# Kernel tuning notes

Measured on AMD Instinct MI355X. Metric: run time of the kernel, lower is better.

## Reference

```python
import jax, jax.numpy as jnp
import numpy as np

N_HEADS = 8


def setup_inputs() -> dict:
    key = jax.random.key(0)
    ks = jax.random.split(key, 6)
    B, U, Lx, Ly = 16, 512, 1024, 1024
    x = jax.random.normal(ks[0], (B, U, Lx), dtype=jnp.float32)
    y = jax.random.normal(ks[1], (B, U, Ly), dtype=jnp.float32)
    xy_mask = jax.random.randint(ks[2], (B, Lx, Ly), 0, 2).astype(jnp.bool_)
    wq = jax.random.normal(ks[3], (U, U), dtype=jnp.float32) * (1.0 / np.sqrt(U))
    wk = jax.random.normal(ks[4], (U, U), dtype=jnp.float32) * (1.0 / np.sqrt(U))
    wo = jax.random.normal(ks[5], (U, U), dtype=jnp.float32) * (1.0 / np.sqrt(U))
    return {"x": x, "y": y, "xy_mask": xy_mask, "wq": wq, "wk": wk, "wo": wo}


def reference(x, y, xy_mask, wq, wk, wo):
    # x: (B, U, Lx), y: (B, U, Ly), xy_mask: (B, Lx, Ly)
    B, U, Lx = x.shape
    Ly = y.shape[2]
    H = N_HEADS
    d = U // H
    scale = 1.0 / (d ** 0.5)

    # 1x1 conv (bias=False) == channel-mixing matmul; weight layout (out, in)
    Q = jnp.einsum('ou,bul->bol', wq, x)   # (B, U, Lx)
    K = jnp.einsum('ou,bul->bol', wk, y)   # (B, U, Ly)

    # split channels into heads (head-major channel order, matching torch.split)
    Qh = Q.reshape(B, H, d, Lx)
    Kh = K.reshape(B, H, d, Ly)

    # ReLU-scored attention with mask (no softmax)
    A = jnp.einsum('bhdx,bhdy->bhxy', Qh, Kh)           # (B, H, Lx, Ly)
    A = jnp.maximum(A, 0.0) * scale
    A = jnp.where(xy_mask[:, None, :, :], A, 0.0)

    C = jnp.einsum('bhxy,bhdy->bhdx', A, Kh).reshape(B, U, Lx)

    # per-row element-count normalization (rows with zero count use 1)
    n_el = jnp.maximum(jnp.sum(xy_mask, axis=2), 1)     # (B, Lx)
    C = C / n_el[:, None, :].astype(x.dtype)

    E = 0.5 * (Q + C)
    return jnp.einsum('ou,bul->bol', wo, E)
```

## Files before the change

kernel.cpp:

```cpp
#include <hip/hip_runtime.h>
#include <stdint.h>
#include <stddef.h>

#define B_  16
#define U_  512
#define LX_ 1024
#define LY_ 1024
#define H_  8
#define D_  64

typedef unsigned short ushort_t;
typedef unsigned int   uint_t;
typedef __bf16 v8bf  __attribute__((ext_vector_type(8)));
typedef float  v16f  __attribute__((ext_vector_type(16)));

__device__ __forceinline__ ushort_t bf16u(float f) {
    uint_t u = __float_as_uint(f);
    uint_t r = (u + 0x7FFFu + ((u >> 16) & 1u)) >> 16;
    return (ushort_t)r;
}
__device__ __forceinline__ float bfu2f(ushort_t u) {
    return __uint_as_float(((uint_t)u) << 16);
}
__device__ __forceinline__ uint_t pkbf16(float f0, float f1) {
    uint_t u0 = __float_as_uint(f0), u1 = __float_as_uint(f1);
    u0 = u0 + 0x7FFFu + ((u0 >> 16) & 1u);
    u1 = u1 + 0x7FFFu + ((u1 >> 16) & 1u);
    return __builtin_amdgcn_perm(u1, u0, 0x07060302u);
}
__device__ __forceinline__ void gload16(const void* g, void* l) {
    auto gp = (const __attribute__((address_space(1))) uint32_t*)(uintptr_t)g;
    auto lp = (__attribute__((address_space(3))) uint32_t*)(uintptr_t)l;
    __builtin_amdgcn_global_load_lds(gp, lp, 16, 0, 0);
}

__global__ void detect_kernel(const uint_t* __restrict__ mask, int* __restrict__ flag) {
    __shared__ int s;
    if (threadIdx.x == 0) s = 0;
    __syncthreads();
    int c = 0;
    for (int i = threadIdx.x; i < 1024; i += 256) c += (mask[i] <= 1u) ? 1 : 0;
    atomicAdd(&s, c);
    __syncthreads();
    if (threadIdx.x == 0) *flag = (s >= 1000) ? 1 : 0;
}

__global__ __launch_bounds__(256) void nelmask_kernel(const void* __restrict__ mask,
                                                      const int* __restrict__ flag,
                                                      float* __restrict__ nel,
                                                      uint_t* __restrict__ mb) {
    int row  = blockIdx.x * 4 + (threadIdx.x >> 6);
    int lane = threadIdx.x & 63;
    const int isInt = *flag;
    const uint8_t* m8  = (const uint8_t*)mask + (size_t)row * LY_;
    const int*     m32 = (const int*)mask + (size_t)row * LY_;
    int cnt = 0;
    for (int yg = 0; yg < LY_ / 64; ++yg) {
        int y = yg * 64 + lane;
        bool p = isInt ? (m32[y] != 0) : (m8[y] != 0);
        unsigned long long bal = __ballot(p);
        if (lane == 0) {
            mb[(size_t)row * 32 + yg * 2]     = (uint_t)bal;
            mb[(size_t)row * 32 + yg * 2 + 1] = (uint_t)(bal >> 32);
            cnt += __popcll(bal);
        }
    }
    if (lane == 0) nel[row] = (float)(cnt > 0 ? cnt : 1);
}

__global__ __launch_bounds__(256) void castw_kernel(const float* __restrict__ w0,
                                                    const float* __restrict__ w1,
                                                    const float* __restrict__ w2,
                                                    ushort_t* __restrict__ o0,
                                                    ushort_t* __restrict__ o1,
                                                    ushort_t* __restrict__ o2) {
    const float* s = blockIdx.y == 0 ? w0 : (blockIdx.y == 1 ? w1 : w2);
    ushort_t*    d = blockIdx.y == 0 ? o0 : (blockIdx.y == 1 ? o1 : o2);
    int i = (blockIdx.x * 256 + threadIdx.x) * 4;
    float4 v = *(const float4*)&s[i];
    ushort4 p;
    p.x = bf16u(v.x); p.y = bf16u(v.y); p.z = bf16u(v.z); p.w = bf16u(v.w);
    *(ushort4*)&d[i] = p;
}

__global__ __launch_bounds__(256) void castT_kernel(const float* __restrict__ X,
                                                    const float* __restrict__ Y,
                                                    ushort_t* __restrict__ XT,
                                                    ushort_t* __restrict__ YT) {
    const int l0 = blockIdx.x * 64;
    const int u0 = blockIdx.y * 64;
    const int b  = blockIdx.z & 15;
    const int sel = blockIdx.z >> 4;
    const float* S = sel ? Y : X;
    ushort_t*  Dst = sel ? YT : XT;
    __shared__ ushort_t T[64][72];
    const int tid = threadIdx.x;
    #pragma unroll
    for (int e = 0; e < 4; ++e) {
        int ci = e * 256 + tid;
        int r = ci >> 4, c4 = (ci & 15) * 4;
        float4 v = *(const float4*)&S[((size_t)(b * U_ + u0 + r) << 10) + l0 + c4];
        T[r][c4 + 0] = bf16u(v.x); T[r][c4 + 1] = bf16u(v.y);
        T[r][c4 + 2] = bf16u(v.z); T[r][c4 + 3] = bf16u(v.w);
    }
    __syncthreads();
    #pragma unroll
    for (int e = 0; e < 2; ++e) {
        int ci = e * 256 + tid;
        int lr = ci >> 3, cc = ci & 7;
        ushort_t tmp[8];
        #pragma unroll
        for (int j = 0; j < 8; ++j) tmp[j] = T[cc * 8 + j][lr];
        *(uint4*)&Dst[((size_t)((b << 10) + l0 + lr)) * U_ + u0 + cc * 8] = *(uint4*)tmp;
    }
}

template <int OUTF32>
__global__ __launch_bounds__(256) void gemm_mfma(const ushort_t* __restrict__ A, size_t aStr,
                                                 const ushort_t* __restrict__ Bm, size_t bStr,
                                                 void* __restrict__ Out, size_t oStr, int ldOut) {
    const int n0 = blockIdx.x * 128;
    const int m0 = blockIdx.y * 128;
    const int b  = blockIdx.z;
    __shared__ __align__(16) ushort_t As[128 * 64];
    __shared__ __align__(16) ushort_t Bs[128 * 64];
    const int tid = threadIdx.x;
    const ushort_t* Ab = A + aStr * b;
    const ushort_t* Bb = Bm + bStr * b;

    const int w = tid >> 6, lane = tid & 63, lo = lane & 31, hi = lane >> 5;
    const int wm = (w >> 1) * 64, wn = (w & 1) * 64;

    v16f acc00, acc01, acc10, acc11;
    #pragma unroll
    for (int i = 0; i < 16; ++i) { acc00[i] = 0.f; acc01[i] = 0.f; acc10[i] = 0.f; acc11[i] = 0.f; }

    for (int kk = 0; kk < 8; ++kk) {
        const int k0 = kk * 64;
        #pragma unroll
        for (int e = 0; e < 4; ++e) {
            int ci = e * 256 + tid;
            int r = ci >> 3, c = ci & 7;
            int g = (c ^ (r & 7)) << 3;
            gload16(&Ab[(size_t)(m0 + r) * U_ + k0 + g], &As[ci * 8]);
            gload16(&Bb[(size_t)(n0 + r) * U_ + k0 + g], &Bs[ci * 8]);
        }
        __syncthreads();
        #pragma unroll
        for (int ks = 0; ks < 4; ++ks) {
            int ch = ks * 2 + hi;
            int rA0 = wm + lo, rA1 = wm + 32 + lo;
            int rB0 = wn + lo, rB1 = wn + 32 + lo;
            v8bf a0 = *(v8bf*)&As[rA0 * 64 + ((ch ^ (rA0 & 7)) << 3)];
            v8bf a1 = *(v8bf*)&As[rA1 * 64 + ((ch ^ (rA1 & 7)) << 3)];
            v8bf b0 = *(v8bf*)&Bs[rB0 * 64 + ((ch ^ (rB0 & 7)) << 3)];
            v8bf b1 = *(v8bf*)&Bs[rB1 * 64 + ((ch ^ (rB1 & 7)) << 3)];
            acc00 = __builtin_amdgcn_mfma_f32_32x32x16_bf16(a0, b0, acc00, 0, 0, 0);
            acc01 = __builtin_amdgcn_mfma_f32_32x32x16_bf16(a0, b1, acc01, 0, 0, 0);
            acc10 = __builtin_amdgcn_mfma_f32_32x32x16_bf16(a1, b0, acc10, 0, 0, 0);
            acc11 = __builtin_amdgcn_mfma_f32_32x32x16_bf16(a1, b1, acc11, 0, 0, 0);
        }
        __syncthreads();
    }

    #pragma unroll
    for (int mi = 0; mi < 2; ++mi) {
        #pragma unroll
        for (int nj = 0; nj < 2; ++nj) {
            v16f c = mi ? (nj ? acc11 : acc10) : (nj ? acc01 : acc00);
            int n = n0 + wn + nj * 32 + lo;
            #pragma unroll
            for (int r = 0; r < 16; ++r) {
                int m = m0 + wm + mi * 32 + (r & 3) + 8 * (r >> 2) + 4 * hi;
                size_t addr = oStr * b + (size_t)m * ldOut + n;
                if (OUTF32) ((float*)Out)[addr] = c[r];
                else        ((ushort_t*)Out)[addr] = bf16u(c[r]);
            }
        }
    }
}

__global__ __launch_bounds__(256) void ktranspose_kernel(const ushort_t* __restrict__ Ka,
                                                         ushort_t* __restrict__ Kb) {
    const int y0 = blockIdx.x * 64;
    const int h  = blockIdx.y;
    const int b  = blockIdx.z;
    __shared__ ushort_t T[64][72];
    const int tid = threadIdx.x;

    #pragma unroll
    for (int e = 0; e < 2; ++e) {
        int idx = e * 256 + tid;
        int d = idx >> 3, c = idx & 7;
        uint4 v = *(const uint4*)&Ka[((size_t)(b * U_ + h * D_ + d) << 10) + y0 + c * 8];
        *(uint4*)&T[d][c * 8] = v;
    }
    __syncthreads();
    #pragma unroll
    for (int e = 0; e < 2; ++e) {
        int idx = e * 256 + tid;
        int yy = idx >> 3, dc = idx & 7;
        ushort_t tmp[8];
        #pragma unroll
        for (int j = 0; j < 8; ++j) tmp[j] = T[dc * 8 + j][yy];
        *(uint4*)&Kb[(((size_t)(b * H_ + h) << 10) + y0 + yy) * D_ + dc * 8] = *(uint4*)tmp;
    }
}

__global__ __launch_bounds__(256, 3) void attn_mfma(const ushort_t* __restrict__ QTg,
                                                    const ushort_t* __restrict__ Ka_g,
                                                    const ushort_t* __restrict__ Kb_g,
                                                    const uint_t* __restrict__ mbits,
                                                    const float* __restrict__ nel,
                                                    ushort_t* __restrict__ ETg) {
    const int tid = threadIdx.x;
    const int id  = blockIdx.x;
    const int bh  = id & 127;
    const int x0g = (id >> 7) * 128;
    const int b = bh >> 3, h = bh & 7;

    __shared__ __align__(16) ushort_t Qt[128 * 64];
    __shared__ __align__(16) ushort_t Kb[64 * 64];
    __shared__ __align__(16) ushort_t Ka[64 * 64];
    __shared__ __align__(16) ushort_t St[128 * 64];

    const int w    = tid >> 6;
    const int lane = tid & 63;
    const int lo   = lane & 31;
    const int hi   = lane >> 5;
    const int yw   = w & 1;
    const int xws  = (w >> 1) * 64;

    const ushort_t* Qsrc = QTg + ((size_t)(b * LX_ + x0g)) * U_ + h * D_;
    #pragma unroll
    for (int e = 0; e < 4; ++e) {
        int ci = e * 256 + tid;
        int r = ci >> 3, c = ci & 7;
        gload16(&Qsrc[(size_t)r * U_ + ((c ^ (r & 7)) << 3)], &Qt[ci * 8]);
    }
    const ushort_t* KaBase = Ka_g + ((size_t)(b * U_ + h * D_)) * LY_;
    const ushort_t* KbBase = Kb_g + ((size_t)(b * H_ + h)) * LY_ * D_;

    __syncthreads();
    v8bf qf0[4], qf1[4];
    {
        int rB0 = xws + lo, rB1 = xws + 32 + lo;
        #pragma unroll
        for (int kt = 0; kt < 4; ++kt) {
            int ch = kt * 2 + hi;
            qf0[kt] = *(v8bf*)&Qt[rB0 * 64 + ((ch ^ (rB0 & 7)) << 3)];
            qf1[kt] = *(v8bf*)&Qt[rB1 * 64 + ((ch ^ (rB1 & 7)) << 3)];
        }
    }

    v16f accC0, accC1;
    #pragma unroll
    for (int i = 0; i < 16; ++i) { accC0[i] = 0.f; accC1[i] = 0.f; }

    const int rowA = yw * 32 + lo;
    const int rB0  = xws + lo, rB1 = xws + 32 + lo;

    for (int y0 = 0; y0 < LY_; y0 += 64) {
        __syncthreads();
        #pragma unroll
        for (int e = 0; e < 2; ++e) {
            int ci = e * 256 + tid;
            int r = ci >> 3, c = ci & 7;
            int g8 = (c ^ (r & 7)) << 3;
            gload16(&KbBase[(size_t)(y0 + r) * D_ + g8], &Kb[ci * 8]);
            gload16(&KaBase[(size_t)r * LY_ + y0 + g8], &Ka[ci * 8]);
        }
        __syncthreads();

        v16f s0, s1;
        #pragma unroll
        for (int i = 0; i < 16; ++i) { s0[i] = 0.f; s1[i] = 0.f; }
        #pragma unroll
        for (int kt = 0; kt < 4; ++kt) {
            int ch = kt * 2 + hi;
            v8bf a = *(v8bf*)&Kb[rowA * 64 + ((ch ^ (rowA & 7)) << 3)];
            s0 = __builtin_amdgcn_mfma_f32_32x32x16_bf16(a, qf0[kt], s0, 0, 0, 0);
            s1 = __builtin_amdgcn_mfma_f32_32x32x16_bf16(a, qf1[kt], s1, 0, 0, 0);
        }
        #pragma unroll
        for (int i = 0; i < 2; ++i) {
            v16f s = i ? s1 : s0;
            int xl = xws + i * 32 + lo;
            uint_t wbits = mbits[((size_t)(b * LX_ + x0g + xl)) * 32 + (y0 >> 5) + yw];
            #pragma unroll
            for (int g = 0; g < 4; ++g) {
                uint_t w2 = wbits >> (g * 8 + 4 * hi);
                float f0 = fmaxf(s[g * 4 + 0], 0.f), f1 = fmaxf(s[g * 4 + 1], 0.f);
                float f2 = fmaxf(s[g * 4 + 2], 0.f), f3 = fmaxf(s[g * 4 + 3], 0.f);
                uint_t m0 = ((w2 & 1u) * 0xFFFFu) | ((w2 & 2u) * 0x7FFF8000u);
                uint_t m1 = (((w2 >> 2) & 1u) * 0xFFFFu) | (((w2 >> 2) & 2u) * 0x7FFF8000u);
                uint2 pk;
                pk.x = pkbf16(f0, f1) & m0;
                pk.y = pkbf16(f2, f3) & m1;
                int yb = yw * 32 + g * 8 + 4 * hi;
                *(uint2*)&St[xl * 64 + (((yb >> 3) ^ (xl & 7)) << 3) + (yb & 7)] = pk;
            }
        }
        __syncthreads();

        #pragma unroll
        for (int kt = 0; kt < 4; ++kt) {
            int ch = kt * 2 + hi;
            v8bf a  = *(v8bf*)&Ka[rowA * 64 + ((ch ^ (rowA & 7)) << 3)];
            v8bf b0 = *(v8bf*)&St[rB0 * 64 + ((ch ^ (rB0 & 7)) << 3)];
            v8bf b1 = *(v8bf*)&St[rB1 * 64 + ((ch ^ (rB1 & 7)) << 3)];
            accC0 = __builtin_amdgcn_mfma_f32_32x32x16_bf16(a, b0, accC0, 0, 0, 0);
            accC1 = __builtin_amdgcn_mfma_f32_32x32x16_bf16(a, b1, accC1, 0, 0, 0);
        }
    }

    __syncthreads();
    ushort_t* Et = St;
    #pragma unroll
    for (int i = 0; i < 2; ++i) {
        v16f c = i ? accC1 : accC0;
        int xl = xws + i * 32 + lo;
        float invn = 0.0625f / nel[b * LX_ + x0g + xl];
        #pragma unroll
        for (int g = 0; g < 4; ++g) {
            int d0 = yw * 32 + g * 8 + 4 * hi;
            int base = xl * 64 + ((((d0 >> 3) ^ (xl & 7)) << 3) | (d0 & 7));
            ushort_t q4[4];
            *(uint2*)q4 = *(const uint2*)&Qt[base];
            ushort_t e4[4];
            #pragma unroll
            for (int r4 = 0; r4 < 4; ++r4) {
                float e = 0.5f * bfu2f(q4[r4]) + c[g * 4 + r4] * invn;
                e4[r4] = bf16u(e);
            }
            *(uint2*)&Et[base] = *(uint2*)e4;
        }
    }
    __syncthreads();
    #pragma unroll
    for (int e = 0; e < 4; ++e) {
        int idx = e * 256 + tid;
        int row = idx >> 3, cc = idx & 7;
        uint4 v = *(const uint4*)&Et[row * 64 + ((cc ^ (row & 7)) << 3)];
        *(uint4*)&ETg[((size_t)(b * LX_ + x0g + row)) * U_ + h * D_ + cc * 8] = v;
    }
}

extern "C" void kernel_launch(void* const* d_in, const int* in_sizes, int n_in,
                              void* d_out, int out_size, void* d_ws, size_t ws_size,
                              hipStream_t stream) {
    const float* x    = (const float*)d_in[0];
    const float* y    = (const float*)d_in[1];
    const void*  mask = d_in[2];
    const float* wq   = (const float*)d_in[3];
    const float* wk   = (const float*)d_in[4];
    const float* wo   = (const float*)d_in[5];

    char* wsb = (char*)d_ws;
    ushort_t* xT    = (ushort_t*)(wsb);
    ushort_t* yT    = (ushort_t*)(wsb + 16777216);
    ushort_t* Ka    = (ushort_t*)(wsb + 33554432);
    ushort_t* wqb   = (ushort_t*)(wsb + 50331648);
    ushort_t* wkb   = (ushort_t*)(wsb + 50855936);
    ushort_t* wob   = (ushort_t*)(wsb + 51380224);
    uint_t*   mbits = (uint_t*)(wsb + 51904512);
    float*    nel   = (float*)(wsb + 54001664);
    int*      flag  = (int*)(wsb + 54067200);
    ushort_t* ET    = xT;
    ushort_t* Kb    = yT;
    ushort_t* QT    = (ushort_t*)d_out;

    detect_kernel<<<1, 256, 0, stream>>>((const uint_t*)mask, flag);
    nelmask_kernel<<<(B_ * LX_) / 4, 256, 0, stream>>>(mask, flag, nel, mbits);
    castw_kernel<<<dim3(U_ * U_ / 1024, 3), 256, 0, stream>>>(wq, wk, wo, wqb, wkb, wob);
    castT_kernel<<<dim3(16, 8, 32), 256, 0, stream>>>(x, y, xT, yT);

    gemm_mfma<0><<<dim3(4, 8, B_), 256, 0, stream>>>(
        xT, (size_t)LX_ * U_, wqb, 0, (void*)QT, (size_t)LX_ * U_, U_);
    gemm_mfma<0><<<dim3(8, 4, B_), 256, 0, stream>>>(
        wkb, 0, yT, (size_t)LY_ * U_, (void*)Ka, (size_t)U_ * LY_, LY_);
    ktranspose_kernel<<<dim3(LY_ / 64, H_, B_), 256, 0, stream>>>(Ka, Kb);
    attn_mfma<<<1024, 256, 0, stream>>>(QT, Ka, Kb, mbits, nel, ET);
    gemm_mfma<1><<<dim3(8, 4, B_), 256, 0, stream>>>(
        wob, 0, ET, (size_t)LX_ * U_, d_out, (size_t)U_ * LX_, LX_);
}
```

Before: 309.5 us.

## Fuse K transpose into K projection GEMM and shrink attention LDS footprint

Replaces the separate K GEMM and transpose kernel with one GEMM that writes both the channel-major Ka and the head-transposed Kb layouts through an LDS staging pass, removing a kernel launch and one full read of Ka. In the attention kernel the score tile now reuses the Q LDS buffer, so occupancy can rise to 4 blocks per CU, and the epilogue re-reads Q from global memory instead of LDS. The ReLU/mask packing switches to truncating bf16 conversion and bitfield-extract masks, which changes rounding of the attention scores slightly. Workspace buffers for Kb and ET are swapped to avoid aliasing with yT, which the new GEMM still reads.

```diff
diff --git a/kernel.cpp b/kernel.cpp
--- a/kernel.cpp
+++ b/kernel.cpp
@@ -13,6 +13,7 @@
 typedef unsigned int   uint_t;
 typedef __bf16 v8bf  __attribute__((ext_vector_type(8)));
 typedef float  v16f  __attribute__((ext_vector_type(16)));
+typedef float  v2f   __attribute__((ext_vector_type(2)));
 
 __device__ __forceinline__ ushort_t bf16u(float f) {
     uint_t u = __float_as_uint(f);
@@ -27,6 +28,9 @@
     u0 = u0 + 0x7FFFu + ((u0 >> 16) & 1u);
     u1 = u1 + 0x7FFFu + ((u1 >> 16) & 1u);
     return __builtin_amdgcn_perm(u1, u0, 0x07060302u);
+}
+__device__ __forceinline__ uint_t pkbf16_trunc(float f0, float f1) {
+    return __builtin_amdgcn_perm(__float_as_uint(f1), __float_as_uint(f0), 0x07060302u);
 }
 __device__ __forceinline__ void gload16(const void* g, void* l) {
     auto gp = (const __attribute__((address_space(1))) uint32_t*)(uintptr_t)g;
@@ -180,34 +184,93 @@
     }
 }
 
-__global__ __launch_bounds__(256) void ktranspose_kernel(const ushort_t* __restrict__ Ka,
-                                                         ushort_t* __restrict__ Kb) {
-    const int y0 = blockIdx.x * 64;
-    const int h  = blockIdx.y;
+__global__ __launch_bounds__(256) void gemm_k(const ushort_t* __restrict__ A,
+                                              const ushort_t* __restrict__ Bm,
+                                              ushort_t* __restrict__ Ka,
+                                              ushort_t* __restrict__ Kb) {
+    const int n0 = blockIdx.x * 128;
+    const int m0 = blockIdx.y * 128;
     const int b  = blockIdx.z;
-    __shared__ ushort_t T[64][72];
+    __shared__ __align__(16) ushort_t SM[128 * 128];
+    ushort_t* As = SM;
+    ushort_t* Bs = SM + 128 * 64;
     const int tid = threadIdx.x;
-
-    #pragma unroll
-    for (int e = 0; e < 2; ++e) {
+    const ushort_t* Bb = Bm + ((size_t)b << 10) * U_;
+
+    const int w = tid >> 6, lane = tid & 63, lo = lane & 31, hi = lane >> 5;
+    const int wm = (w >> 1) * 64, wn = (w & 1) * 64;
+
+    v16f acc00, acc01, acc10, acc11;
+    #pragma unroll
+    for (int i = 0; i < 16; ++i) { acc00[i] = 0.f; acc01[i] = 0.f; acc10[i] = 0.f; acc11[i] = 0.f; }
+
+    for (int kk = 0; kk < 8; ++kk) {
+        const int k0 = kk * 64;
+        #pragma unroll
+        for (int e = 0; e < 4; ++e) {
+            int ci = e * 256 + tid;
+            int r = ci >> 3, c = ci & 7;
+            int g = (c ^ (r & 7)) << 3;
+            gload16(&A[(size_t)(m0 + r) * U_ + k0 + g], &As[ci * 8]);
+            gload16(&Bb[(size_t)(n0 + r) * U_ + k0 + g], &Bs[ci * 8]);
+        }
+        __syncthreads();
+        #pragma unroll
+        for (int ks = 0; ks < 4; ++ks) {
+            int ch = ks * 2 + hi;
+            int rA0 = wm + lo, rA1 = wm + 32 + lo;
+            int rB0 = wn + lo, rB1 = wn + 32 + lo;
+            v8bf a0 = *(v8bf*)&As[rA0 * 64 + ((ch ^ (rA0 & 7)) << 3)];
+            v8bf a1 = *(v8bf*)&As[rA1 * 64 + ((ch ^ (rA1 & 7)) << 3)];
+            v8bf b0 = *(v8bf*)&Bs[rB0 * 64 + ((ch ^ (rB0 & 7)) << 3)];
+            v8bf b1 = *(v8bf*)&Bs[rB1 * 64 + ((ch ^ (rB1 & 7)) << 3)];
+            acc00 = __builtin_amdgcn_mfma_f32_32x32x16_bf16(a0, b0, acc00, 0, 0, 0);
+            acc01 = __builtin_amdgcn_mfma_f32_32x32x16_bf16(a0, b1, acc01, 0, 0, 0);
+            acc10 = __builtin_amdgcn_mfma_f32_32x32x16_bf16(a1, b0, acc10, 0, 0, 0);
+            acc11 = __builtin_amdgcn_mfma_f32_32x32x16_bf16(a1, b1, acc11, 0, 0, 0);
+        }
+        __syncthreads();
+    }
+
+    #pragma unroll
+    for (int mi = 0; mi < 2; ++mi) {
+        #pragma unroll
+        for (int nj = 0; nj < 2; ++nj) {
+            v16f c = mi ? (nj ? acc11 : acc10) : (nj ? acc01 : acc00);
+            int y_l = wn + nj * 32 + lo;
+            int n = n0 + y_l;
+            #pragma unroll
+            for (int r = 0; r < 16; ++r) {
+                int m = m0 + wm + mi * 32 + (r & 3) + 8 * (r >> 2) + 4 * hi;
+                Ka[((size_t)(b * U_ + m) << 10) + n] = bf16u(c[r]);
+            }
+            #pragma unroll
+            for (int q = 0; q < 4; ++q) {
+                int u4 = wm + mi * 32 + 8 * q + 4 * hi;
+                int c4 = u4 >> 2;
+                int col = ((c4 + (y_l & 31)) & 31) * 4;
+                uint2 pk;
+                pk.x = pkbf16(c[4 * q + 0], c[4 * q + 1]);
+                pk.y = pkbf16(c[4 * q + 2], c[4 * q + 3]);
+                *(uint2*)&SM[y_l * 128 + col] = pk;
+            }
+        }
+    }
+    __syncthreads();
+    #pragma unroll
+    for (int e = 0; e < 8; ++e) {
         int idx = e * 256 + tid;
-        int d = idx >> 3, c = idx & 7;
-        uint4 v = *(const uint4*)&Ka[((size_t)(b * U_ + h * D_ + d) << 10) + y0 + c * 8];
-        *(uint4*)&T[d][c * 8] = v;
-    }
-    __syncthreads();
-    #pragma unroll
-    for (int e = 0; e < 2; ++e) {
-        int idx = e * 256 + tid;
-        int yy = idx >> 3, dc = idx & 7;
-        ushort_t tmp[8];
-        #pragma unroll
-        for (int j = 0; j < 8; ++j) tmp[j] = T[dc * 8 + j][yy];
-        *(uint4*)&Kb[(((size_t)(b * H_ + h) << 10) + y0 + yy) * D_ + dc * 8] = *(uint4*)tmp;
-    }
-}
-
-__global__ __launch_bounds__(256, 3) void attn_mfma(const ushort_t* __restrict__ QTg,
+        int row = idx >> 4, cc = idx & 15;
+        uint2 a = *(const uint2*)&SM[row * 128 + (((2 * cc)     + (row & 31) & 31)) * 4];
+        uint2 bq = *(const uint2*)&SM[row * 128 + (((2 * cc + 1) + (row & 31) & 31)) * 4];
+        uint4 v = make_uint4(a.x, a.y, bq.x, bq.y);
+        int ug = m0 + cc * 8;
+        int h = ug >> 6, d = ug & 63;
+        *(uint4*)&Kb[(((size_t)(b * H_ + h) << 10) + n0 + row) * D_ + d] = v;
+    }
+}
+
+__global__ __launch_bounds__(256, 4) void attn_mfma(const ushort_t* __restrict__ QTg,
                                                     const ushort_t* __restrict__ Ka_g,
                                                     const ushort_t* __restrict__ Kb_g,
                                                     const uint_t* __restrict__ mbits,
@@ -219,10 +282,9 @@
     const int x0g = (id >> 7) * 128;
     const int b = bh >> 3, h = bh & 7;
 
-    __shared__ __align__(16) ushort_t Qt[128 * 64];
+    __shared__ __align__(16) ushort_t QS[128 * 64];
     __shared__ __align__(16) ushort_t Kb[64 * 64];
     __shared__ __align__(16) ushort_t Ka[64 * 64];
-    __shared__ __align__(16) ushort_t St[128 * 64];
 
     const int w    = tid >> 6;
     const int lane = tid & 63;
@@ -236,21 +298,19 @@
     for (int e = 0; e < 4; ++e) {
         int ci = e * 256 + tid;
         int r = ci >> 3, c = ci & 7;
-        gload16(&Qsrc[(size_t)r * U_ + ((c ^ (r & 7)) << 3)], &Qt[ci * 8]);
+        gload16(&Qsrc[(size_t)r * U_ + ((c ^ (r & 7)) << 3)], &QS[ci * 8]);
     }
     const ushort_t* KaBase = Ka_g + ((size_t)(b * U_ + h * D_)) * LY_;
     const ushort_t* KbBase = Kb_g + ((size_t)(b * H_ + h)) * LY_ * D_;
 
     __syncthreads();
     v8bf qf0[4], qf1[4];
-    {
-        int rB0 = xws + lo, rB1 = xws + 32 + lo;
-        #pragma unroll
-        for (int kt = 0; kt < 4; ++kt) {
-            int ch = kt * 2 + hi;
-            qf0[kt] = *(v8bf*)&Qt[rB0 * 64 + ((ch ^ (rB0 & 7)) << 3)];
-            qf1[kt] = *(v8bf*)&Qt[rB1 * 64 + ((ch ^ (rB1 & 7)) << 3)];
-        }
+    const int rB0 = xws + lo, rB1 = xws + 32 + lo;
+    #pragma unroll
+    for (int kt = 0; kt < 4; ++kt) {
+        int ch = kt * 2 + hi;
+        qf0[kt] = *(v8bf*)&QS[rB0 * 64 + ((ch ^ (rB0 & 7)) << 3)];
+        qf1[kt] = *(v8bf*)&QS[rB1 * 64 + ((ch ^ (rB1 & 7)) << 3)];
     }
 
     v16f accC0, accC1;
@@ -258,7 +318,7 @@
     for (int i = 0; i < 16; ++i) { accC0[i] = 0.f; accC1[i] = 0.f; }
 
     const int rowA = yw * 32 + lo;
-    const int rB0  = xws + lo, rB1 = xws + 32 + lo;
+    ushort_t* St = QS;
 
     for (int y0 = 0; y0 < LY_; y0 += 64) {
         __syncthreads();
@@ -290,13 +350,15 @@
             #pragma unroll
             for (int g = 0; g < 4; ++g) {
                 uint_t w2 = wbits >> (g * 8 + 4 * hi);
-                float f0 = fmaxf(s[g * 4 + 0], 0.f), f1 = fmaxf(s[g * 4 + 1], 0.f);
-                float f2 = fmaxf(s[g * 4 + 2], 0.f), f3 = fmaxf(s[g * 4 + 3], 0.f);
-                uint_t m0 = ((w2 & 1u) * 0xFFFFu) | ((w2 & 2u) * 0x7FFF8000u);
-                uint_t m1 = (((w2 >> 2) & 1u) * 0xFFFFu) | (((w2 >> 2) & 2u) * 0x7FFF8000u);
+                v2f p01 = __builtin_elementwise_max((v2f){s[g * 4 + 0], s[g * 4 + 1]}, (v2f){0.f, 0.f});
+                v2f p23 = __builtin_elementwise_max((v2f){s[g * 4 + 2], s[g * 4 + 3]}, (v2f){0.f, 0.f});
+                uint_t m0 = (uint_t)__builtin_amdgcn_sbfe(w2, 0, 1);
+                uint_t m1 = (uint_t)__builtin_amdgcn_sbfe(w2, 1, 1);
+                uint_t m2 = (uint_t)__builtin_amdgcn_sbfe(w2, 2, 1);
+                uint_t m3 = (uint_t)__builtin_amdgcn_sbfe(w2, 3, 1);
                 uint2 pk;
-                pk.x = pkbf16(f0, f1) & m0;
-                pk.y = pkbf16(f2, f3) & m1;
+                pk.x = pkbf16_trunc(p01[0], p01[1]) & __builtin_amdgcn_perm(m1, m0, 0x07060302u);
+                pk.y = pkbf16_trunc(p23[0], p23[1]) & __builtin_amdgcn_perm(m3, m2, 0x07060302u);
                 int yb = yw * 32 + g * 8 + 4 * hi;
                 *(uint2*)&St[xl * 64 + (((yb >> 3) ^ (xl & 7)) << 3) + (yb & 7)] = pk;
             }
@@ -315,7 +377,7 @@
     }
 
     __syncthreads();
-    ushort_t* Et = St;
+    ushort_t* Et = QS;
     #pragma unroll
     for (int i = 0; i < 2; ++i) {
         v16f c = i ? accC1 : accC0;
@@ -324,16 +386,16 @@
         #pragma unroll
         for (int g = 0; g < 4; ++g) {
             int d0 = yw * 32 + g * 8 + 4 * hi;
-            int base = xl * 64 + ((((d0 >> 3) ^ (xl & 7)) << 3) | (d0 & 7));
+            uint2 qv = *(const uint2*)&Qsrc[(size_t)xl * U_ + d0];
             ushort_t q4[4];
-            *(uint2*)q4 = *(const uint2*)&Qt[base];
+            *(uint2*)q4 = qv;
             ushort_t e4[4];
             #pragma unroll
             for (int r4 = 0; r4 < 4; ++r4) {
                 float e = 0.5f * bfu2f(q4[r4]) + c[g * 4 + r4] * invn;
                 e4[r4] = bf16u(e);
             }
-            *(uint2*)&Et[base] = *(uint2*)e4;
+            *(uint2*)&Et[xl * 64 + ((((d0 >> 3) ^ (xl & 7)) << 3) | (d0 & 7))] = *(uint2*)e4;
         }
     }
     __syncthreads();
@@ -366,8 +428,8 @@
     uint_t*   mbits = (uint_t*)(wsb + 51904512);
     float*    nel   = (float*)(wsb + 54001664);
     int*      flag  = (int*)(wsb + 54067200);
-    ushort_t* ET    = xT;
-    ushort_t* Kb    = yT;
+    ushort_t* Kb    = xT;
+    ushort_t* ET    = yT;
     ushort_t* QT    = (ushort_t*)d_out;
 
     detect_kernel<<<1, 256, 0, stream>>>((const uint_t*)mask, flag);
@@ -377,9 +439,7 @@
 
     gemm_mfma<0><<<dim3(4, 8, B_), 256, 0, stream>>>(
         xT, (size_t)LX_ * U_, wqb, 0, (void*)QT, (size_t)LX_ * U_, U_);
-    gemm_mfma<0><<<dim3(8, 4, B_), 256, 0, stream>>>(
-        wkb, 0, yT, (size_t)LY_ * U_, (void*)Ka, (size_t)U_ * LY_, LY_);
-    ktranspose_kernel<<<dim3(LY_ / 64, H_, B_), 256, 0, stream>>>(Ka, Kb);
+    gemm_k<<<dim3(8, 4, B_), 256, 0, stream>>>(wkb, yT, Ka, Kb);
     attn_mfma<<<1024, 256, 0, stream>>>(QT, Ka, Kb, mbits, nel, ET);
     gemm_mfma<1><<<dim3(8, 4, B_), 256, 0, stream>>>(
         wob, 0, ET, (size_t)LX_ * U_, d_out, (size_t)U_ * LX_, LX_);
```

Result: slower. 324.8 us (+5.0%).
